# Optimization experiments

Hardware: AMD Instinct MI355X
Metric: run time of the kernel (lower is better)

## Reference

```python
import jax, jax.numpy as jnp
import numpy as np


def setup_inputs() -> dict:
    key = jax.random.key(0)
    k1, k2 = jax.random.split(key)
    a_bar = jax.random.normal(k1, (32, 512, 512), dtype=jnp.float32)
    b_bar = jax.random.normal(k2, (32, 512, 512), dtype=jnp.float32)
    return {"a_bar": a_bar, "b_bar": b_bar}


def reference(a_bar, b_bar):
    # e[b,i,j] = <a_bar[b,i,:], b_bar[b,j,:]>
    e = jnp.einsum("bid,bjd->bij", a_bar, b_bar)
    # a_tilde: row softmax (over j) then weighted sum of b rows
    attn_a = jax.nn.softmax(e, axis=2)            # [B, Sa, Sb]
    a_tilde = jnp.einsum("bij,bjd->bid", attn_a, b_bar)
    # b_tilde: column softmax (over i), transposed, times a_bar
    attn_b = jax.nn.softmax(e, axis=1)            # [B, Sa, Sb]
    b_tilde = jnp.einsum("bij,bid->bjd", attn_b, a_bar)
    m_a = jnp.concatenate([a_bar, a_tilde, a_bar - a_tilde, a_bar * a_tilde], axis=-1)
    m_b = jnp.concatenate([b_bar, b_tilde, b_bar - b_tilde, b_bar * b_tilde], axis=-1)
    return (m_a, m_b)
```

## Files before the change

### kernel.cpp

```cpp
#include <hip/hip_runtime.h>
#include <hip/hip_bf16.h>
#include <math.h>

#define B_   32
#define S_   512
#define SxS  (S_ * S_)
#define LOG2E 1.4426950408889634f

using frag_ab = __attribute__((ext_vector_type(8))) short;
using frag_cd = __attribute__((ext_vector_type(4))) float;

__device__ inline short f2bf(float x) {
    __hip_bfloat16 h = __float2bfloat16(x);
    return *reinterpret_cast<short*>(&h);
}
__device__ inline float bf2f(short s) {
    __hip_bfloat16 h = *reinterpret_cast<__hip_bfloat16*>(&s);
    return __bfloat162float(h);
}

__device__ __forceinline__ void async16(const short* g, short* l) {
    __builtin_amdgcn_global_load_lds(
        (const __attribute__((address_space(1))) void*)g,
        (__attribute__((address_space(3))) void*)l,
        16, 0, 0);
}

__global__ __launch_bounds__(256) void k_prep(const float* __restrict__ A,
                                              const float* __restrict__ Bm,
                                              short* __restrict__ PA,
                                              short* __restrict__ PB,
                                              short* __restrict__ At,
                                              short* __restrict__ Bt)
{
    const int z   = blockIdx.z;
    const int b   = z & 31;
    const int isB = z >> 5;
    const float* X = (isB ? Bm : A) + (size_t)b * SxS;
    short* P  = (isB ? PB : PA) + (size_t)b * (S_ * 1024);
    short* Xt = (isB ? Bt : At) + (size_t)b * SxS;
    const float scale = isB ? 1.0f : LOG2E;

    const int i0 = blockIdx.y * 64, d0 = blockIdx.x * 64;

    __shared__ short T[64][68];

    const int sl = threadIdx.x & 7;
    const int il = threadIdx.x >> 3;

    #pragma unroll
    for (int p = 0; p < 2; ++p) {
        const int i    = il + 32 * p;
        const int rowg = i0 + i;
        const float* src = X + (size_t)rowg * S_ + d0 + sl * 8;
        const float4 v0 = *(const float4*)(src);
        const float4 v1 = *(const float4*)(src + 4);

        T[sl * 8 + 0][i] = f2bf(v0.x); T[sl * 8 + 1][i] = f2bf(v0.y);
        T[sl * 8 + 2][i] = f2bf(v0.z); T[sl * 8 + 3][i] = f2bf(v0.w);
        T[sl * 8 + 4][i] = f2bf(v1.x); T[sl * 8 + 5][i] = f2bf(v1.y);
        T[sl * 8 + 6][i] = f2bf(v1.z); T[sl * 8 + 7][i] = f2bf(v1.w);

        const float xs[8] = {v0.x, v0.y, v0.z, v0.w, v1.x, v1.y, v1.z, v1.w};
        frag_ab hi, lo;
        #pragma unroll
        for (int j = 0; j < 8; ++j) {
            const float x = xs[j] * scale;
            const short h = f2bf(x);
            hi[j] = h;
            lo[j] = f2bf(x - bf2f(h));
        }
        const int W = (d0 >> 5) + (sl >> 2);
        const int q = sl & 3;
        short* base = P + (size_t)rowg * 1024 + W * 64;
        *(frag_ab*)(base + (((2 * q)     ^ (rowg & 7)) * 8)) = hi;
        *(frag_ab*)(base + (((2 * q + 1) ^ (rowg & 7)) * 8)) = lo;
    }
    __syncthreads();

    const int r = threadIdx.x >> 4, c = threadIdx.x & 15;
    #pragma unroll
    for (int p = 0; p < 4; ++p) {
        const int d = r + p * 16;
        *(short4*)(Xt + (size_t)(d0 + d) * S_ + i0 + c * 4) = *(short4*)&T[d][c * 4];
    }
}

__global__ __launch_bounds__(256) void k_gemm_e(const short* __restrict__ PA,
                                                const short* __restrict__ PB,
                                                float* __restrict__ E,
                                                float* __restrict__ Et)
{
    const int lin     = blockIdx.x + (blockIdx.y << 2) + (blockIdx.z << 4);
    const int logical = ((lin & 7) << 6) + (lin >> 3);
    const int b  = logical >> 4;
    const int i0 = ((logical >> 2) & 3) * 128;
    const int j0 = (logical & 3) * 128;

    const short* Ab = PA + (size_t)b * (S_ * 1024);
    const short* Bb = PB + (size_t)b * (S_ * 1024);
    float* Eb  = E  + (size_t)b * SxS;
    float* Etb = Et + (size_t)b * SxS;

    __shared__ __align__(16) short As[128][64];
    __shared__ __align__(16) short Bs[128][64];

    const int tid  = threadIdx.x;
    const int wave = tid >> 6, lane = tid & 63;
    const int wr   = wave >> 1, wc = wave & 1;
    const int q    = lane >> 4, m = lane & 15;
    const int srow = lane >> 3, schunk = lane & 7;

    frag_cd zero = {0.f, 0.f, 0.f, 0.f};
    frag_cd acc[4][4];
    #pragma unroll
    for (int i = 0; i < 4; ++i)
        #pragma unroll
        for (int j = 0; j < 4; ++j) acc[i][j] = zero;

    for (int k0 = 0; k0 < S_; k0 += 32) {
        const int W = k0 >> 5;
        __syncthreads();
        #pragma unroll
        for (int p = 0; p < 4; ++p) {
            const int seg    = wave * 4 + p;
            const int rowg_a = i0 + seg * 8 + srow;
            const int rowg_b = j0 + seg * 8 + srow;
            async16(Ab + (size_t)rowg_a * 1024 + W * 64 + schunk * 8, &As[seg * 8][0]);
            async16(Bb + (size_t)rowg_b * 1024 + W * 64 + schunk * 8, &Bs[seg * 8][0]);
        }
        __syncthreads();

        frag_ab ah[4], al[4], bh[4], bl[4];
        #pragma unroll
        for (int t = 0; t < 4; ++t) {
            const int ra = wr * 64 + t * 16 + m;
            const int rb = wc * 64 + t * 16 + m;
            ah[t] = *(const frag_ab*)&As[ra][((2 * q)     ^ (ra & 7)) * 8];
            al[t] = *(const frag_ab*)&As[ra][((2 * q + 1) ^ (ra & 7)) * 8];
            bh[t] = *(const frag_ab*)&Bs[rb][((2 * q)     ^ (rb & 7)) * 8];
            bl[t] = *(const frag_ab*)&Bs[rb][((2 * q + 1) ^ (rb & 7)) * 8];
        }
        #pragma unroll
        for (int mt = 0; mt < 4; ++mt)
            #pragma unroll
            for (int nt = 0; nt < 4; ++nt) {
                acc[mt][nt] = __builtin_amdgcn_mfma_f32_16x16x32_bf16(ah[mt], bh[nt], acc[mt][nt], 0, 0, 0);
                acc[mt][nt] = __builtin_amdgcn_mfma_f32_16x16x32_bf16(ah[mt], bl[nt], acc[mt][nt], 0, 0, 0);
                acc[mt][nt] = __builtin_amdgcn_mfma_f32_16x16x32_bf16(al[mt], bh[nt], acc[mt][nt], 0, 0, 0);
            }
    }

    #pragma unroll
    for (int mt = 0; mt < 4; ++mt)
        #pragma unroll
        for (int nt = 0; nt < 4; ++nt) {
            const int rb  = i0 + wr * 64 + mt * 16 + q * 4;
            const int col = j0 + wc * 64 + nt * 16 + m;
            float4 v = make_float4(acc[mt][nt][0], acc[mt][nt][1],
                                   acc[mt][nt][2], acc[mt][nt][3]);
            Eb[(size_t)(rb + 0) * S_ + col] = v.x;
            Eb[(size_t)(rb + 1) * S_ + col] = v.y;
            Eb[(size_t)(rb + 2) * S_ + col] = v.z;
            Eb[(size_t)(rb + 3) * S_ + col] = v.w;
            *(float4*)(Etb + (size_t)col * S_ + rb) = v;
        }
}

__global__ __launch_bounds__(256) void k_rowstats(const float* __restrict__ E,
                                                  const float* __restrict__ Et,
                                                  float* __restrict__ rmax,
                                                  float* __restrict__ rinv,
                                                  float* __restrict__ cmax,
                                                  float* __restrict__ cinv)
{
    const float* src = blockIdx.y ? Et : E;
    float* pm = blockIdx.y ? cmax : rmax;
    float* pi = blockIdx.y ? cinv : rinv;

    const int row  = blockIdx.x * 4 + (threadIdx.x >> 6);
    const int lane = threadIdx.x & 63;
    const float* er = src + (size_t)row * S_;

    float4 v0 = *(const float4*)(er + lane * 4);
    float4 v1 = *(const float4*)(er + 256 + lane * 4);

    float m = fmaxf(fmaxf(fmaxf(v0.x, v0.y), fmaxf(v0.z, v0.w)),
                    fmaxf(fmaxf(v1.x, v1.y), fmaxf(v1.z, v1.w)));
    #pragma unroll
    for (int off = 32; off >= 1; off >>= 1)
        m = fmaxf(m, __shfl_xor(m, off));

    float s = exp2f(v0.x - m) + exp2f(v0.y - m)
            + exp2f(v0.z - m) + exp2f(v0.w - m)
            + exp2f(v1.x - m) + exp2f(v1.y - m)
            + exp2f(v1.z - m) + exp2f(v1.w - m);
    #pragma unroll
    for (int off = 32; off >= 1; off >>= 1)
        s += __shfl_xor(s, off);

    if (lane == 0) { pm[row] = m; pi[row] = 1.0f / s; }
}

__global__ __launch_bounds__(256) void k_pv(const float* __restrict__ E,
                                            const float* __restrict__ Et,
                                            const float* __restrict__ rmx_,
                                            const float* __restrict__ rin_,
                                            const float* __restrict__ cmx_,
                                            const float* __restrict__ cin_,
                                            const short* __restrict__ At,
                                            const short* __restrict__ Bt,
                                            const float* __restrict__ A,
                                            const float* __restrict__ Bm,
                                            float* __restrict__ Ma,
                                            float* __restrict__ Mb)
{
    const int lin     = blockIdx.x + (blockIdx.y << 2) + (blockIdx.z << 4);
    const int logical = ((lin & 7) << 7) + (lin >> 3);
    const int zz   = logical >> 4;
    const int side = zz >> 5, b = zz & 31;
    const int r0 = ((logical >> 2) & 3) * 128, d0 = (logical & 3) * 128;

    const float* Eb  = (side ? Et : E) + (size_t)b * SxS;
    const float* rmb = (side ? cmx_ : rmx_) + b * S_;
    const float* rib = (side ? cin_ : rin_) + b * S_;
    const short* Vb  = (side ? At : Bt) + (size_t)b * SxS;
    const float* Xb  = (side ? Bm : A) + (size_t)b * SxS;
    float* Ob = (side ? Mb : Ma) + (size_t)b * S_ * 2048;

    __shared__ __align__(16) short Ps[128][40], Vs[128][40];

    const int tid  = threadIdx.x;
    const int kc   = tid & 7, lr = tid >> 3;
    const int kb   = tid & 3, dr = tid >> 2;
    const int wave = tid >> 6, lane = tid & 63;
    const int wr   = wave >> 1, wc = wave & 1;
    const int q    = lane >> 4, m = lane & 15;

    float rml[4];
    #pragma unroll
    for (int p = 0; p < 4; ++p) rml[p] = rmb[r0 + lr + 32 * p];

    frag_cd zero = {0.f, 0.f, 0.f, 0.f};
    frag_cd acc[4][4];
    #pragma unroll
    for (int i = 0; i < 4; ++i)
        #pragma unroll
        for (int j = 0; j < 4; ++j) acc[i][j] = zero;

    for (int k0 = 0; k0 < S_; k0 += 32) {
        float4 ev[4];
        #pragma unroll
        for (int p = 0; p < 4; ++p)
            ev[p] = *(const float4*)(Eb + (size_t)(r0 + lr + 32 * p) * S_ + k0 + kc * 4);
        frag_ab vv[2];
        #pragma unroll
        for (int p = 0; p < 2; ++p)
            vv[p] = *(const frag_ab*)(Vb + (size_t)(d0 + dr + 64 * p) * S_ + k0 + kb * 8);

        __syncthreads();
        #pragma unroll
        for (int p = 0; p < 4; ++p) {
            short4 pv;
            pv.x = f2bf(exp2f(ev[p].x - rml[p]));
            pv.y = f2bf(exp2f(ev[p].y - rml[p]));
            pv.z = f2bf(exp2f(ev[p].z - rml[p]));
            pv.w = f2bf(exp2f(ev[p].w - rml[p]));
            *(short4*)&Ps[lr + 32 * p][kc * 4] = pv;
        }
        #pragma unroll
        for (int p = 0; p < 2; ++p)
            *(frag_ab*)&Vs[dr + 64 * p][kb * 8] = vv[p];
        __syncthreads();

        frag_ab af[4], bfr[4];
        #pragma unroll
        for (int t = 0; t < 4; ++t) {
            af[t]  = *(const frag_ab*)&Ps[wr * 64 + t * 16 + m][q * 8];
            bfr[t] = *(const frag_ab*)&Vs[wc * 64 + t * 16 + m][q * 8];
        }
        #pragma unroll
        for (int mt = 0; mt < 4; ++mt)
            #pragma unroll
            for (int nt = 0; nt < 4; ++nt)
                acc[mt][nt] = __builtin_amdgcn_mfma_f32_16x16x32_bf16(af[mt], bfr[nt], acc[mt][nt], 0, 0, 0);
    }

    #pragma unroll
    for (int mt = 0; mt < 4; ++mt)
        #pragma unroll
        for (int nt = 0; nt < 4; ++nt) {
            const int rb  = r0 + wr * 64 + mt * 16 + q * 4;
            const int col = d0 + wc * 64 + nt * 16 + m;
            #pragma unroll
            for (int r = 0; r < 4; ++r) {
                const int row = rb + r;
                const float s  = rib[row];
                const float at = acc[mt][nt][r] * s;
                const float xv = Xb[(size_t)row * S_ + col];
                float* o = Ob + (size_t)row * 2048 + col;
                o[0]    = xv;
                o[512]  = at;
                o[1024] = xv - at;
                o[1536] = xv * at;
            }
        }
}

extern "C" void kernel_launch(void* const* d_in, const int* in_sizes, int n_in,
                              void* d_out, int out_size, void* d_ws, size_t ws_size,
                              hipStream_t stream)
{
    const float* A  = (const float*)d_in[0];
    const float* Bm = (const float*)d_in[1];
    float* Ma = (float*)d_out;
    float* Mb = Ma + (size_t)B_ * S_ * 2048;

    float* E    = (float*)d_ws;
    float* Et   = E + (size_t)B_ * SxS;
    short* At   = (short*)(Et + (size_t)B_ * SxS);
    short* Bt   = At + (size_t)B_ * SxS;
    float* rmax = (float*)(Bt + (size_t)B_ * SxS);
    float* rinv = rmax + B_ * S_;
    float* cmax = rinv + B_ * S_;
    float* cinv = cmax + B_ * S_;

    short* PA = (short*)d_out;
    short* PB = PA + (size_t)B_ * S_ * 1024;

    k_prep    <<<dim3(8, 8, 64),  256, 0, stream>>>(A, Bm, PA, PB, At, Bt);
    k_gemm_e  <<<dim3(4, 4, 32),  256, 0, stream>>>(PA, PB, E, Et);
    k_rowstats<<<dim3(4096, 2),   256, 0, stream>>>(E, Et, rmax, rinv, cmax, cinv);
    k_pv      <<<dim3(4, 4, 64),  256, 0, stream>>>(E, Et, rmax, rinv, cmax, cinv,
                                                    At, Bt, A, Bm, Ma, Mb);
}
```

Baseline: 480.3 us.

## Precompute bf16 softmax numerators in stats kernel and async-load them in PV GEMM

The row/column stats kernel now also computes exp2(e - max), packs it to bf16 in a swizzled layout and writes it in place over the fp32 E/Et buffers. The PV kernel no longer recomputes exponentials from fp32 E. It streams pre-swizzled bf16 P and V tiles with global_load_lds async copies and uses 64-wide K steps. The prep kernel writes V in a matching XOR-swizzled layout. This cuts PV-side global traffic in half and removes redundant exp work, at the cost of an extra write pass in the stats kernel. In-place aliasing of E as short storage relies on each row being read before it is overwritten within the same wave.

```diff
diff --git a/kernel.cpp b/kernel.cpp
--- a/kernel.cpp
+++ b/kernel.cpp
@@ -30,20 +30,20 @@
                                               const float* __restrict__ Bm,
                                               short* __restrict__ PA,
                                               short* __restrict__ PB,
-                                              short* __restrict__ At,
-                                              short* __restrict__ Bt)
+                                              short* __restrict__ Va,
+                                              short* __restrict__ Vb)
 {
     const int z   = blockIdx.z;
     const int b   = z & 31;
     const int isB = z >> 5;
     const float* X = (isB ? Bm : A) + (size_t)b * SxS;
     short* P  = (isB ? PB : PA) + (size_t)b * (S_ * 1024);
-    short* Xt = (isB ? Bt : At) + (size_t)b * SxS;
+    short* Vp = (isB ? Vb : Va) + (size_t)b * SxS;
     const float scale = isB ? 1.0f : LOG2E;
 
     const int i0 = blockIdx.y * 64, d0 = blockIdx.x * 64;
 
-    __shared__ short T[64][68];
+    __shared__ short T[64][72];
 
     const int sl = threadIdx.x & 7;
     const int il = threadIdx.x >> 3;
@@ -78,11 +78,13 @@
     }
     __syncthreads();
 
-    const int r = threadIdx.x >> 4, c = threadIdx.x & 15;
-    #pragma unroll
-    for (int p = 0; p < 4; ++p) {
-        const int d = r + p * 16;
-        *(short4*)(Xt + (size_t)(d0 + d) * S_ + i0 + c * 4) = *(short4*)&T[d][c * 4];
+    const int pc = threadIdx.x & 7, dl = threadIdx.x >> 3;
+    #pragma unroll
+    for (int p = 0; p < 2; ++p) {
+        const int d  = dl + 32 * p;
+        const int dg = d0 + d;
+        frag_ab t = *(const frag_ab*)&T[d][pc * 8];
+        *(frag_ab*)(Vp + (size_t)dg * 512 + i0 + ((pc ^ (dg & 7)) * 8)) = t;
     }
 }
 
@@ -167,49 +169,50 @@
         }
 }
 
-__global__ __launch_bounds__(256) void k_rowstats(const float* __restrict__ E,
-                                                  const float* __restrict__ Et,
-                                                  float* __restrict__ rmax,
-                                                  float* __restrict__ rinv,
-                                                  float* __restrict__ cmax,
-                                                  float* __restrict__ cinv)
-{
-    const float* src = blockIdx.y ? Et : E;
-    float* pm = blockIdx.y ? cmax : rmax;
-    float* pi = blockIdx.y ? cinv : rinv;
+__global__ __launch_bounds__(256) void k_softp(float* __restrict__ E,
+                                               float* __restrict__ Et,
+                                               float* __restrict__ rinv,
+                                               float* __restrict__ cinv)
+{
+    float* buf = blockIdx.y ? Et : E;
+    float* piv = blockIdx.y ? cinv : rinv;
 
     const int row  = blockIdx.x * 4 + (threadIdx.x >> 6);
     const int lane = threadIdx.x & 63;
-    const float* er = src + (size_t)row * S_;
-
-    float4 v0 = *(const float4*)(er + lane * 4);
-    float4 v1 = *(const float4*)(er + 256 + lane * 4);
-
-    float m = fmaxf(fmaxf(fmaxf(v0.x, v0.y), fmaxf(v0.z, v0.w)),
-                    fmaxf(fmaxf(v1.x, v1.y), fmaxf(v1.z, v1.w)));
-    #pragma unroll
-    for (int off = 32; off >= 1; off >>= 1)
-        m = fmaxf(m, __shfl_xor(m, off));
-
-    float s = exp2f(v0.x - m) + exp2f(v0.y - m)
-            + exp2f(v0.z - m) + exp2f(v0.w - m)
-            + exp2f(v1.x - m) + exp2f(v1.y - m)
-            + exp2f(v1.z - m) + exp2f(v1.w - m);
-    #pragma unroll
-    for (int off = 32; off >= 1; off >>= 1)
-        s += __shfl_xor(s, off);
-
-    if (lane == 0) { pm[row] = m; pi[row] = 1.0f / s; }
+    float* er = buf + (size_t)row * S_;
+
+    const float4 v0 = *(const float4*)(er + lane * 8);
+    const float4 v1 = *(const float4*)(er + lane * 8 + 4);
+    const float xs[8] = {v0.x, v0.y, v0.z, v0.w, v1.x, v1.y, v1.z, v1.w};
+
+    float m = xs[0];
+    #pragma unroll
+    for (int j = 1; j < 8; ++j) m = fmaxf(m, xs[j]);
+    #pragma unroll
+    for (int off = 32; off >= 1; off >>= 1) m = fmaxf(m, __shfl_xor(m, off));
+
+    float p[8], s = 0.f;
+    #pragma unroll
+    for (int j = 0; j < 8; ++j) { p[j] = exp2f(xs[j] - m); s += p[j]; }
+    #pragma unroll
+    for (int off = 32; off >= 1; off >>= 1) s += __shfl_xor(s, off);
+
+    frag_ab out;
+    #pragma unroll
+    for (int j = 0; j < 8; ++j) out[j] = f2bf(p[j]);
+
+    short* pr = (short*)buf + (size_t)row * 1024;
+    const int W = lane >> 3, slt = (lane & 7) ^ (row & 7);
+    *(frag_ab*)(pr + W * 64 + slt * 8) = out;
+    if (lane == 0) piv[row] = 1.0f / s;
 }
 
 __global__ __launch_bounds__(256) void k_pv(const float* __restrict__ E,
                                             const float* __restrict__ Et,
-                                            const float* __restrict__ rmx_,
                                             const float* __restrict__ rin_,
-                                            const float* __restrict__ cmx_,
                                             const float* __restrict__ cin_,
-                                            const short* __restrict__ At,
-                                            const short* __restrict__ Bt,
+                                            const short* __restrict__ Va,
+                                            const short* __restrict__ Vb,
                                             const float* __restrict__ A,
                                             const float* __restrict__ Bm,
                                             float* __restrict__ Ma,
@@ -221,25 +224,20 @@
     const int side = zz >> 5, b = zz & 31;
     const int r0 = ((logical >> 2) & 3) * 128, d0 = (logical & 3) * 128;
 
-    const float* Eb  = (side ? Et : E) + (size_t)b * SxS;
-    const float* rmb = (side ? cmx_ : rmx_) + b * S_;
+    const short* Pb  = (const short*)(side ? Et : E) + (size_t)b * (S_ * 1024);
     const float* rib = (side ? cin_ : rin_) + b * S_;
-    const short* Vb  = (side ? At : Bt) + (size_t)b * SxS;
+    const short* Vp  = (side ? Va : Vb) + (size_t)b * SxS;
     const float* Xb  = (side ? Bm : A) + (size_t)b * SxS;
     float* Ob = (side ? Mb : Ma) + (size_t)b * S_ * 2048;
 
-    __shared__ __align__(16) short Ps[128][40], Vs[128][40];
+    __shared__ __align__(16) short Ps[128][64];
+    __shared__ __align__(16) short Vs[128][64];
 
     const int tid  = threadIdx.x;
-    const int kc   = tid & 7, lr = tid >> 3;
-    const int kb   = tid & 3, dr = tid >> 2;
     const int wave = tid >> 6, lane = tid & 63;
     const int wr   = wave >> 1, wc = wave & 1;
     const int q    = lane >> 4, m = lane & 15;
-
-    float rml[4];
-    #pragma unroll
-    for (int p = 0; p < 4; ++p) rml[p] = rmb[r0 + lr + 32 * p];
+    const int srow = lane >> 3, schunk = lane & 7;
 
     frag_cd zero = {0.f, 0.f, 0.f, 0.f};
     frag_cd acc[4][4];
@@ -248,42 +246,35 @@
         #pragma unroll
         for (int j = 0; j < 4; ++j) acc[i][j] = zero;
 
-    for (int k0 = 0; k0 < S_; k0 += 32) {
-        float4 ev[4];
-        #pragma unroll
-        for (int p = 0; p < 4; ++p)
-            ev[p] = *(const float4*)(Eb + (size_t)(r0 + lr + 32 * p) * S_ + k0 + kc * 4);
-        frag_ab vv[2];
-        #pragma unroll
-        for (int p = 0; p < 2; ++p)
-            vv[p] = *(const frag_ab*)(Vb + (size_t)(d0 + dr + 64 * p) * S_ + k0 + kb * 8);
-
+    for (int k0 = 0; k0 < S_; k0 += 64) {
+        const int W = k0 >> 6;
         __syncthreads();
         #pragma unroll
         for (int p = 0; p < 4; ++p) {
-            short4 pv;
-            pv.x = f2bf(exp2f(ev[p].x - rml[p]));
-            pv.y = f2bf(exp2f(ev[p].y - rml[p]));
-            pv.z = f2bf(exp2f(ev[p].z - rml[p]));
-            pv.w = f2bf(exp2f(ev[p].w - rml[p]));
-            *(short4*)&Ps[lr + 32 * p][kc * 4] = pv;
-        }
-        #pragma unroll
-        for (int p = 0; p < 2; ++p)
-            *(frag_ab*)&Vs[dr + 64 * p][kb * 8] = vv[p];
+            const int seg = wave * 4 + p;
+            async16(Pb + (size_t)(r0 + seg * 8 + srow) * 1024 + W * 64 + schunk * 8,
+                    &Ps[seg * 8][0]);
+            async16(Vp + (size_t)(d0 + seg * 8 + srow) * 512  + W * 64 + schunk * 8,
+                    &Vs[seg * 8][0]);
+        }
         __syncthreads();
 
-        frag_ab af[4], bfr[4];
-        #pragma unroll
-        for (int t = 0; t < 4; ++t) {
-            af[t]  = *(const frag_ab*)&Ps[wr * 64 + t * 16 + m][q * 8];
-            bfr[t] = *(const frag_ab*)&Vs[wc * 64 + t * 16 + m][q * 8];
-        }
-        #pragma unroll
-        for (int mt = 0; mt < 4; ++mt)
+        #pragma unroll
+        for (int kk = 0; kk < 2; ++kk) {
+            frag_ab af[4], bfr[4];
             #pragma unroll
-            for (int nt = 0; nt < 4; ++nt)
-                acc[mt][nt] = __builtin_amdgcn_mfma_f32_16x16x32_bf16(af[mt], bfr[nt], acc[mt][nt], 0, 0, 0);
+            for (int t = 0; t < 4; ++t) {
+                const int ra = wr * 64 + t * 16 + m;
+                const int rb = wc * 64 + t * 16 + m;
+                af[t]  = *(const frag_ab*)&Ps[ra][(((kk * 4 + q) ^ (ra & 7)) * 8)];
+                bfr[t] = *(const frag_ab*)&Vs[rb][(((kk * 4 + q) ^ (rb & 7)) * 8)];
+            }
+            #pragma unroll
+            for (int mt = 0; mt < 4; ++mt)
+                #pragma unroll
+                for (int nt = 0; nt < 4; ++nt)
+                    acc[mt][nt] = __builtin_amdgcn_mfma_f32_16x16x32_bf16(af[mt], bfr[nt], acc[mt][nt], 0, 0, 0);
+        }
     }
 
     #pragma unroll
@@ -295,8 +286,7 @@
             #pragma unroll
             for (int r = 0; r < 4; ++r) {
                 const int row = rb + r;
-                const float s  = rib[row];
-                const float at = acc[mt][nt][r] * s;
+                const float at = acc[mt][nt][r] * rib[row];
                 const float xv = Xb[(size_t)row * S_ + col];
                 float* o = Ob + (size_t)row * 2048 + col;
                 o[0]    = xv;
@@ -318,19 +308,17 @@
 
     float* E    = (float*)d_ws;
     float* Et   = E + (size_t)B_ * SxS;
-    short* At   = (short*)(Et + (size_t)B_ * SxS);
-    short* Bt   = At + (size_t)B_ * SxS;
-    float* rmax = (float*)(Bt + (size_t)B_ * SxS);
-    float* rinv = rmax + B_ * S_;
-    float* cmax = rinv + B_ * S_;
-    float* cinv = cmax + B_ * S_;
+    short* Va   = (short*)(Et + (size_t)B_ * SxS);
+    short* Vb   = Va + (size_t)B_ * SxS;
+    float* rinv = (float*)(Vb + (size_t)B_ * SxS);
+    float* cinv = rinv + B_ * S_;
 
     short* PA = (short*)d_out;
     short* PB = PA + (size_t)B_ * S_ * 1024;
 
-    k_prep    <<<dim3(8, 8, 64),  256, 0, stream>>>(A, Bm, PA, PB, At, Bt);
-    k_gemm_e  <<<dim3(4, 4, 32),  256, 0, stream>>>(PA, PB, E, Et);
-    k_rowstats<<<dim3(4096, 2),   256, 0, stream>>>(E, Et, rmax, rinv, cmax, cinv);
-    k_pv      <<<dim3(4, 4, 64),  256, 0, stream>>>(E, Et, rmax, rinv, cmax, cinv,
-                                                    At, Bt, A, Bm, Ma, Mb);
-}
+    k_prep  <<<dim3(8, 8, 64), 256, 0, stream>>>(A, Bm, PA, PB, Va, Vb);
+    k_gemm_e<<<dim3(4, 4, 32), 256, 0, stream>>>(PA, PB, E, Et);
+    k_softp <<<dim3(4096, 2),  256, 0, stream>>>(E, Et, rinv, cinv);
+    k_pv    <<<dim3(4, 4, 64), 256, 0, stream>>>(E, Et, rinv, cinv,
+                                                 Va, Vb, A, Bm, Ma, Mb);
+}
```

Measured after the change: 469.6 us. -2.2%, faster.
